# Kernel tuning notes

Measured on AMD Instinct MI355X. Metric: run time of the kernel, lower is better.

Reference implementation:

```python
import jax, jax.numpy as jnp
import numpy as np

B, N, QN, C, H = 4, 1024, 512, 1024, 16
D = C // H  # head_dim = 64


def setup_inputs() -> dict:
    key = jax.random.key(0)
    ks = jax.random.split(key, 8)
    w = lambda k, shape: jax.random.normal(k, shape, jnp.float32) * 0.02
    return dict(
        x=jax.random.normal(ks[0], (B, N, C), jnp.float32),
        query=jax.random.normal(ks[1], (B, QN, C), jnp.float32),
        w_qkv=w(ks[2], (3 * C, C)),        # self.qkv (no bias)
        w_kv=w(ks[3], (2 * C, C)),         # self.to_query_kv (no bias)
        w_qlin=w(ks[4], (3 * C, C)),       # self.query_linear (no bias)
        gate=jnp.zeros((1, H, 1, 1), jnp.float32),  # zero-initialized gate param
        w_proj=w(ks[5], (C, C)),
        b_proj=jnp.zeros((C,), jnp.float32),
        w_qproj=w(ks[6], (C, C)),
        b_qproj=jnp.zeros((C,), jnp.float32),
    )


def _sdpa(q, k, v, scale):
    # q,k,v: [B,H,S,D]; standard softmax attention (attn_mask=None, p=0)
    s = jnp.einsum('bhqd,bhkd->bhqk', q, k) * scale
    return jnp.einsum('bhqk,bhkd->bhqd', jax.nn.softmax(s, axis=-1), v)


def reference(x, query, w_qkv, w_kv, w_qlin, gate, w_proj, b_proj, w_qproj, b_qproj):
    scale = 1.0 / np.sqrt(D)
    # qkv on x -> [3,B,H,N,D]
    qkv = (x @ w_qkv.T).reshape(B, N, 3, H, D).transpose(2, 0, 3, 1, 4)
    q, k, v = qkv[0], qkv[1], qkv[2]
    # kv for cross path computed from ORIGINAL x (before self-attn), as in torch code
    kv = (x @ w_kv.T).reshape(B, N, 2, H, D).transpose(2, 0, 3, 1, 4)
    xk0, xv0 = kv[0], kv[1]
    # self-attention on x (x_mask=None)
    x_attn = _sdpa(q, k, v, scale)  # [B,H,N,D]
    # query qkv -> [3,B,H,QN,D]
    qq3 = (query @ w_qlin.T).reshape(B, QN, 3, H, D).transpose(2, 0, 3, 1, 4)
    qq, qk, qv = qq3[0], qq3[1], qq3[2]
    xk = jnp.concatenate([xk0, qk], axis=2)  # [B,H,N+QN,D]
    xv = jnp.concatenate([xv0, qv], axis=2)
    scores = jnp.einsum('bhqd,bhkd->bhqk', qq, xk) * scale  # [B,H,QN,N+QN]
    # split softmax with tanh-gated first segment (mask=None; dropout p=0)
    gated = jnp.concatenate(
        [jnp.tanh(gate) * jax.nn.softmax(scores[..., :N], axis=-1),
         jax.nn.softmax(scores[..., N:], axis=-1)], axis=-1)
    q_attn = jnp.einsum('bhqk,bhkd->bhqd', gated, xv)  # [B,H,QN,D]
    x_out = x_attn.transpose(0, 2, 1, 3).reshape(B, N, C) @ w_proj.T + b_proj
    q_out = q_attn.transpose(0, 2, 1, 3).reshape(B, QN, C) @ w_qproj.T + b_qproj
    return (x_out, q_out)
```

## Files before the change

### kernel.cpp

```cpp
#include <hip/hip_runtime.h>


using bf16 = __bf16;
typedef __bf16 bf16x4 __attribute__((ext_vector_type(4)));
typedef __bf16 bf16x8 __attribute__((ext_vector_type(8)));
typedef float  f32x4  __attribute__((ext_vector_type(4)));
typedef float  f32x16 __attribute__((ext_vector_type(16)));
typedef unsigned int u32x4 __attribute__((ext_vector_type(4)));

#define MFMA16(a, b, c) __builtin_amdgcn_mfma_f32_16x16x32_bf16((a), (b), (c), 0, 0, 0)
#define MFMA32(a, b, c) __builtin_amdgcn_mfma_f32_32x32x16_bf16((a), (b), (c), 0, 0, 0)

__device__ __forceinline__ int swz128(int row) { return ((row ^ (row >> 3)) & 7) << 4; }

__device__ __forceinline__ void gl_lds16(const void* g, void* l) {
  __builtin_amdgcn_global_load_lds(
      (const __attribute__((address_space(1))) unsigned int*)g,
      (__attribute__((address_space(3))) unsigned int*)l, 16, 0, 0);
}

__device__ __forceinline__ unsigned pack2(float a, float b) {
  unsigned short ua = __builtin_bit_cast(unsigned short, (bf16)a);
  unsigned short ub = __builtin_bit_cast(unsigned short, (bf16)b);
  return (unsigned)ua | ((unsigned)ub << 16);
}

__device__ __forceinline__ float exp2_fast(float x) {
  float r;
  asm("v_exp_f32 %0, %1" : "=v"(r) : "v"(x));
  return r;
}

#define WAITV(N) asm volatile("s_waitcnt vmcnt(" #N ")" ::: "memory")
#define RAW_BAR() do { __builtin_amdgcn_s_barrier(); asm volatile("" ::: "memory"); } while (0)

__global__ void k_cast_all(const float* __restrict__ s0, const float* __restrict__ s1,
                           const float* __restrict__ s2, const float* __restrict__ s3,
                           const float* __restrict__ s4, const float* __restrict__ s5,
                           const float* __restrict__ s6, bf16* __restrict__ dst) {
  constexpr size_t MM = 1u << 20;
  constexpr size_t o1 = 4 * MM, o2 = 6 * MM, o3 = 9 * MM, o4 = 11 * MM,
                   o5 = 14 * MM, o6 = 15 * MM, total = 16 * MM;
  size_t stride = (size_t)gridDim.x * blockDim.x * 8;
  for (size_t i = ((size_t)blockIdx.x * blockDim.x + threadIdx.x) * 8; i < total; i += stride) {
    const float* s; size_t loc;
    if (i < o1)      { s = s0; loc = i; }
    else if (i < o2) { s = s1; loc = i - o1; }
    else if (i < o3) { s = s2; loc = i - o2; }
    else if (i < o4) { s = s3; loc = i - o3; }
    else if (i < o5) { s = s4; loc = i - o4; }
    else if (i < o6) { s = s5; loc = i - o5; }
    else             { s = s6; loc = i - o6; }
    float4 a = *(const float4*)(s + loc);
    float4 b = *(const float4*)(s + loc + 4);
    bf16x8 o;
    o[0] = (bf16)a.x; o[1] = (bf16)a.y; o[2] = (bf16)a.z; o[3] = (bf16)a.w;
    o[4] = (bf16)b.x; o[5] = (bf16)b.y; o[6] = (bf16)b.z; o[7] = (bf16)b.w;
    *(bf16x8*)(dst + i) = o;
  }
}

__global__ __launch_bounds__(512, 2)
void k_gemm_big(const bf16* __restrict__ xb, const bf16* __restrict__ qb,
                const bf16* __restrict__ wqkvb, const bf16* __restrict__ wqlinb,
                bf16* __restrict__ XK, bf16* __restrict__ VTs, bf16* __restrict__ VT0,
                bf16* __restrict__ QQK, bf16* __restrict__ VTq) {
  constexpr int K = 1024, NK = 32;
  __shared__ bf16 As[3 * 256 * 32];
  __shared__ bf16 Bs[3 * 256 * 32];
  const int tid = threadIdx.x;
  const int lane = tid & 63, w = tid >> 6;
  const int wm = w >> 2, wn = w & 3;
  const int r0 = lane & 15, kg = lane >> 4;
  const int bid = ((int)blockIdx.x & 7) * 52 + ((int)blockIdx.x >> 3);
  int grp, tm, tn;
  const bf16 *Ap, *Bp;
  if (bid < 320) { grp = 0; tm = (bid / 20) * 256; tn = (bid % 20) * 256; Ap = xb; Bp = wqkvb; }
  else { grp = 1; int t = bid - 320; tm = (t / 12) * 256; tn = (t % 12) * 256; Ap = qb; Bp = wqlinb; }

  auto stage = [&](int step, int bi) {
    const int kk = step * 32;
#pragma unroll
    for (int j = 0; j < 2; j++) {
      int c = j * 512 + tid;
      int row = c >> 2, kb = c & 3;
      int sg = (kb ^ ((row >> 1) & 3)) * 8;
      gl_lds16(Ap + (size_t)(tm + row) * K + kk + sg, (char*)As + bi * 16384 + c * 16);
    }
#pragma unroll
    for (int j = 0; j < 2; j++) {
      int c = j * 512 + tid;
      int row = c >> 2, kb = c & 3;
      int sg = (kb ^ ((row >> 1) & 3)) * 8;
      gl_lds16(Bp + (size_t)(tn + row) * K + kk + sg, (char*)Bs + bi * 16384 + c * 16);
    }
  };

  f32x4 acc[8][4] = {};
  stage(0, 0);
  stage(1, 1);
  WAITV(4);
  RAW_BAR();

  for (int t = 0; t < NK; t++) {
    const int bi = t % 3;
    const bool more = (t + 2 < NK);
    if (more) stage(t + 2, (t + 2) % 3);
    const char* Ab = (const char*)As + bi * 16384;
    const char* Bb = (const char*)Bs + bi * 16384;
    bf16x8 af[8], bfv[4];
#pragma unroll
    for (int mf = 0; mf < 8; mf++) {
      int row = wm * 128 + mf * 16 + r0;
      af[mf] = *(const bf16x8*)(Ab + row * 64 + ((kg ^ ((row >> 1) & 3)) << 4));
    }
#pragma unroll
    for (int nf = 0; nf < 4; nf++) {
      int row = wn * 64 + nf * 16 + r0;
      bfv[nf] = *(const bf16x8*)(Bb + row * 64 + ((kg ^ ((row >> 1) & 3)) << 4));
    }
    __builtin_amdgcn_s_setprio(1);
#pragma unroll
    for (int mf = 0; mf < 8; mf++)
#pragma unroll
      for (int nf = 0; nf < 4; nf++)
        acc[mf][nf] = MFMA16(af[mf], bfv[nf], acc[mf][nf]);
    __builtin_amdgcn_s_setprio(0);
    if (more) { WAITV(4); } else { WAITV(0); }
    RAW_BAR();
  }

#pragma unroll
  for (int mf = 0; mf < 8; mf++) {
    const int rowb = tm + wm * 128 + mf * 16 + kg * 4;
#pragma unroll
    for (int nf = 0; nf < 4; nf++) {
      const int coln = tn + wn * 64 + nf * 16 + r0;
      bool rm; int rmcol = coln, vbase = 0, tokb = 10, rs_ = 3072;
      bf16* vt = VTs;
      bf16* rmp = XK;
      if (grp == 0) {
        if (tn < 2048)      { rm = true; }
        else if (tn < 3072) { rm = false; vbase = 2048; vt = VTs; }
        else if (tn < 4096) { rm = true; rmcol = coln - 1024; }
        else                { rm = false; vbase = 4096; vt = VT0; }
      } else {
        rs_ = 2048; tokb = 9; rmp = QQK;
        if (tn < 2048) { rm = true; }
        else           { rm = false; vbase = 2048; vt = VTq; }
      }
      if (rm) {
#pragma unroll
        for (int j = 0; j < 4; j++)
          rmp[(size_t)(rowb + j) * rs_ + rmcol] = (bf16)acc[mf][nf][j];
      } else {
        int dg = coln - vbase, h_ = dg >> 6, dd = dg & 63;
        int bq = rowb >> tokb, tok = rowb & ((1 << tokb) - 1);
        bf16x4 wv;
#pragma unroll
        for (int j = 0; j < 4; j++) wv[j] = (bf16)acc[mf][nf][j];
        *(bf16x4*)(vt + (((size_t)((bq * 16 + h_) * 64 + dd)) << tokb) + tok) = wv;
      }
    }
  }
}

__global__ __launch_bounds__(256)
void k_gemm_proj(const bf16* __restrict__ A, const bf16* __restrict__ B0,
                 const bf16* __restrict__ B1, const float* __restrict__ bias0,
                 const float* __restrict__ bias1, float* __restrict__ OUT) {
  constexpr int K = 1024, N = 1024;
  __shared__ bf16 As[128 * 64];
  __shared__ bf16 Bs[128 * 64];
  const int tid = threadIdx.x;
  const int lane = tid & 63, w = tid >> 6;
  const int wr = w >> 1, wc = w & 1;
  const int nbx = N / 128;
  const int bid = ((int)blockIdx.x & 7) * ((int)gridDim.x >> 3) + ((int)blockIdx.x >> 3);
  const int tm = (bid / nbx) * 128, tn = (bid % nbx) * 128;
  const int r0 = lane & 15, kg = lane >> 4;
  const bf16* Bp = (tm < 4096) ? B0 : B1;
  const float* bias = (tm < 4096) ? bias0 : bias1;
  f32x4 acc[4][4] = {};
  for (int kk = 0; kk < K; kk += 64) {
#pragma unroll
    for (int i = 0; i < 4; i++) {
      int c = i * 256 + tid;
      int row = c >> 3, kb = c & 7;
      int sb = (kb ^ ((row ^ (row >> 3)) & 7)) * 8;
      gl_lds16(A + (size_t)(tm + row) * K + kk + sb, (char*)As + c * 16);
      gl_lds16(Bp + (size_t)(tn + row) * K + kk + sb, (char*)Bs + c * 16);
    }
    __syncthreads();
#pragma unroll
    for (int ks = 0; ks < 2; ks++) {
      bf16x8 af[4], bfv[4];
#pragma unroll
      for (int f = 0; f < 4; f++) {
        int rowa = wr * 64 + f * 16 + r0;
        af[f] = *(const bf16x8*)((const char*)As +
                                 ((rowa * 128 + ks * 64 + kg * 16) ^ swz128(rowa)));
        int rowb = wc * 64 + f * 16 + r0;
        bfv[f] = *(const bf16x8*)((const char*)Bs +
                                  ((rowb * 128 + ks * 64 + kg * 16) ^ swz128(rowb)));
      }
#pragma unroll
      for (int mf = 0; mf < 4; mf++)
#pragma unroll
        for (int nf = 0; nf < 4; nf++)
          acc[mf][nf] = MFMA16(af[mf], bfv[nf], acc[mf][nf]);
    }
    __syncthreads();
  }
#pragma unroll
  for (int mf = 0; mf < 4; mf++)
#pragma unroll
    for (int j = 0; j < 4; j++) {
      int row = tm + wr * 64 + mf * 16 + kg * 4 + j;
#pragma unroll
      for (int nf = 0; nf < 4; nf++) {
        int col = tn + wc * 64 + nf * 16 + r0;
        OUT[(size_t)row * 1024 + col] = acc[mf][nf][j] + bias[col];
      }
    }
}

template<int NT>
__device__ __forceinline__ void attn_pass32(
    const bf16* __restrict__ Kg, int kRS,
    const bf16* __restrict__ VTg, int vRS,
    int ntiles, const bf16x8* qf, bf16* Ks, bf16* Vt,
    f32x16* o, float& m, float& rs) {
  const int tid = threadIdx.x;
  const int lane = tid & 63;
  const int lq = lane & 31, kg2 = lane >> 5;

  auto stage = [&](int t) {
    bf16* kd = Ks + (t % 3) * 4096;
    bf16* vd = Vt + (t % 3) * 4096;
    const bf16* kt = Kg + (size_t)t * 64 * kRS;
#pragma unroll
    for (int i = 0; i < 512 / NT; i++) {
      int c = i * NT + tid;
      int r = c >> 3, kb = c & 7;
      int sb = (kb ^ ((r ^ (r >> 3)) & 7)) * 8;
      gl_lds16(kt + (size_t)r * kRS + sb, (char*)kd + c * 16);
    }
#pragma unroll
    for (int i = 0; i < 512 / NT; i++) {
      int c = i * NT + tid;
      int r = c >> 3, kb = c & 7;
      int sb = (kb ^ ((r ^ (r >> 3)) & 7)) * 8;
      gl_lds16(VTg + (size_t)r * vRS + t * 64 + sb, (char*)vd + c * 16);
    }
  };

  stage(0);
  stage(1);
  WAITV(4);
  RAW_BAR();

  for (int t = 0; t < ntiles; t++) {
    const char* KsC = (const char*)(Ks + (t % 3) * 4096);
    const char* VtC = (const char*)(Vt + (t % 3) * 4096);
    const bool more = (t + 2 < ntiles);
    if (more) stage(t + 2);

    f32x16 s[2];
    s[0] = (f32x16)0.f; s[1] = (f32x16)0.f;
    __builtin_amdgcn_s_setprio(1);
#pragma unroll
    for (int kb = 0; kb < 2; kb++) {
      int row = kb * 32 + lq;
#pragma unroll
      for (int dw = 0; dw < 4; dw++) {
        bf16x8 kf = *(const bf16x8*)(KsC + ((row * 128 + dw * 32 + kg2 * 16) ^ swz128(row)));
        s[kb] = MFMA32(kf, qf[dw], s[kb]);
      }
    }
    __builtin_amdgcn_s_setprio(0);

    float vmax = s[0][0];
#pragma unroll
    for (int j = 1; j < 16; j++) vmax = fmaxf(vmax, s[0][j]);
#pragma unroll
    for (int j = 0; j < 16; j++) vmax = fmaxf(vmax, s[1][j]);
    vmax = fmaxf(vmax, __shfl_xor(vmax, 32, 64));
    if (__any(vmax > m + 11.5f)) {
      float mn = fmaxf(m, vmax);
      float fac = exp2_fast(m - mn);
      m = mn;
      rs *= fac;
#pragma unroll
      for (int j = 0; j < 16; j++) {
        int rowq = (j & 3) + 8 * (j >> 2) + 4 * kg2;
        float fj = __shfl(fac, rowq, 64);
        o[0][j] *= fj;
        o[1][j] *= fj;
      }
    }
    float tsum = 0.f;
    f32x16 p[2];
#pragma unroll
    for (int kb = 0; kb < 2; kb++)
#pragma unroll
      for (int j = 0; j < 16; j++) {
        float pv = exp2_fast(s[kb][j] - m);
        p[kb][j] = pv;
        tsum += pv;
      }
    tsum += __shfl_xor(tsum, 32, 64);
    rs += tsum;

    unsigned pk[2][4][2];
#pragma unroll
    for (int kb = 0; kb < 2; kb++)
#pragma unroll
      for (int n = 0; n < 4; n++) {
        pk[kb][n][0] = pack2(p[kb][4 * n + 0], p[kb][4 * n + 1]);
        pk[kb][n][1] = pack2(p[kb][4 * n + 2], p[kb][4 * n + 3]);
      }

#pragma unroll
    for (int w = 0; w < 4; w++) {
      const int kb = w >> 1, wb = w & 1;
      unsigned pushA = kg2 ? pk[kb][2 * wb][0] : pk[kb][2 * wb + 1][0];
      unsigned pushB = kg2 ? pk[kb][2 * wb][1] : pk[kb][2 * wb + 1][1];
      unsigned rcvA = __shfl_xor(pushA, 32, 64);
      unsigned rcvB = __shfl_xor(pushB, 32, 64);
      u32x4 fu;
      fu[0] = kg2 ? rcvA : pk[kb][2 * wb][0];
      fu[1] = kg2 ? rcvB : pk[kb][2 * wb][1];
      fu[2] = kg2 ? pk[kb][2 * wb + 1][0] : rcvA;
      fu[3] = kg2 ? pk[kb][2 * wb + 1][1] : rcvB;
      bf16x8 pfrag = __builtin_bit_cast(bf16x8, fu);
      __builtin_amdgcn_s_setprio(1);
#pragma unroll
      for (int db = 0; db < 2; db++) {
        int d = db * 32 + lq;
        bf16x8 vf = *(const bf16x8*)(VtC + ((d * 128 + w * 32 + kg2 * 16) ^ swz128(d)));
        o[db] = MFMA32(pfrag, vf, o[db]);
      }
      __builtin_amdgcn_s_setprio(0);
    }

    if (more) { WAITV(4); } else { WAITV(0); }
    RAW_BAR();
  }
}

__global__ __launch_bounds__(256)
void k_attn(const bf16* __restrict__ XK, const bf16* __restrict__ QQK,
            const bf16* __restrict__ VTs, const bf16* __restrict__ VT0,
            const bf16* __restrict__ VTq, const float* __restrict__ gate,
            bf16* __restrict__ xat, bf16* __restrict__ qat) {
  __shared__ bf16 Ks[3 * 4096], Vt[3 * 4096];
  const int pb = blockIdx.x;
  const int bid = (pb & 7) * 96 + (pb >> 3);
  const int bh = bid / 12, r = bid % 12;
  const int b = bh >> 4, h = bh & 15;
  const int tid = threadIdx.x, lane = tid & 63, wv = tid >> 6;
  const int lq = lane & 31, kg2 = lane >> 5;
  constexpr float QS = 0.125f * 1.44269504088896f;

  if (r < 8) {
    const int qtok = b * 1024 + r * 128 + wv * 32;
    bf16x8 qf[4];
#pragma unroll
    for (int dw = 0; dw < 4; dw++) {
      qf[dw] = *(const bf16x8*)(XK + (size_t)(qtok + lq) * 3072 + h * 64 + dw * 16 + kg2 * 8);
#pragma unroll
      for (int e = 0; e < 8; e++) qf[dw][e] = (bf16)((float)qf[dw][e] * QS);
    }
    f32x16 o[2];
    o[0] = (f32x16)0.f; o[1] = (f32x16)0.f;
    float m = -__builtin_inff(), rs = 0.f;
    attn_pass32<256>(XK + (size_t)(b * 1024) * 3072 + 1024 + h * 64, 3072,
                     VTs + (size_t)bh * 64 * 1024, 1024,
                     16, qf, Ks, Vt, o, m, rs);
#pragma unroll
    for (int j = 0; j < 16; j++) {
      int rowq = (j & 3) + 8 * (j >> 2) + 4 * kg2;
      float rsj = __shfl(rs, rowq, 64);
      size_t base = (size_t)(qtok + rowq) * 1024 + h * 64;
      xat[base + lq] = (bf16)(o[0][j] / rsj);
      xat[base + 32 + lq] = (bf16)(o[1][j] / rsj);
    }
  } else {
    const int qt = r - 8;
    const int qtok = b * 512 + qt * 128 + wv * 32;
    bf16x8 qf[4];
#pragma unroll
    for (int dw = 0; dw < 4; dw++) {
      qf[dw] = *(const bf16x8*)(QQK + (size_t)(qtok + lq) * 2048 + h * 64 + dw * 16 + kg2 * 8);
#pragma unroll
      for (int e = 0; e < 8; e++) qf[dw][e] = (bf16)((float)qf[dw][e] * QS);
    }
    const float g = tanhf(gate[h]);
    unsigned pka[2][8] = {};
    f32x16 o[2];
    o[0] = (f32x16)0.f; o[1] = (f32x16)0.f;
    float m, rs;
    if (g != 0.0f) {
      m = -__builtin_inff(); rs = 0.f;
      attn_pass32<256>(XK + (size_t)(b * 1024) * 3072 + 2048 + h * 64, 3072,
                       VT0 + (size_t)bh * 64 * 1024, 1024,
                       16, qf, Ks, Vt, o, m, rs);
#pragma unroll
      for (int j2 = 0; j2 < 8; j2++) {
        int j0 = 2 * j2;
        int rq0 = (j0 & 3) + 8 * (j0 >> 2) + 4 * kg2;
        float ra = __shfl(rs, rq0, 64);
        float rb = __shfl(rs, rq0 + 1, 64);
        pka[0][j2] = pack2(g * o[0][j0] / ra, g * o[0][j0 + 1] / rb);
        pka[1][j2] = pack2(g * o[1][j0] / ra, g * o[1][j0 + 1] / rb);
      }
      o[0] = (f32x16)0.f; o[1] = (f32x16)0.f;
    }
    m = -__builtin_inff(); rs = 0.f;
    attn_pass32<256>(QQK + (size_t)(b * 512) * 2048 + 1024 + h * 64, 2048,
                     VTq + (size_t)bh * 64 * 512, 512,
                     8, qf, Ks, Vt, o, m, rs);
#pragma unroll
    for (int j = 0; j < 16; j++) {
      int rowq = (j & 3) + 8 * (j >> 2) + 4 * kg2;
      float rsj = __shfl(rs, rowq, 64);
      size_t base = (size_t)(qtok + rowq) * 1024 + h * 64;
      unsigned wa = pka[0][j >> 1], wb = pka[1][j >> 1];
      unsigned short ua = (j & 1) ? (unsigned short)(wa >> 16) : (unsigned short)(wa & 0xffffu);
      unsigned short ub = (j & 1) ? (unsigned short)(wb >> 16) : (unsigned short)(wb & 0xffffu);
      float a0 = (float)__builtin_bit_cast(bf16, ua);
      float a1 = (float)__builtin_bit_cast(bf16, ub);
      qat[base + lq] = (bf16)(o[0][j] / rsj + a0);
      qat[base + 32 + lq] = (bf16)(o[1][j] / rsj + a1);
    }
  }
}

extern "C" void kernel_launch(void* const* d_in, const int* in_sizes, int n_in,
                              void* d_out, int out_size, void* d_ws, size_t ws_size,
                              hipStream_t stream) {
  (void)in_sizes; (void)n_in; (void)out_size; (void)ws_size;
  const float* x       = (const float*)d_in[0];
  const float* query   = (const float*)d_in[1];
  const float* w_qkv   = (const float*)d_in[2];
  const float* w_kv    = (const float*)d_in[3];
  const float* w_qlin  = (const float*)d_in[4];
  const float* gate    = (const float*)d_in[5];
  const float* w_proj  = (const float*)d_in[6];
  const float* b_proj  = (const float*)d_in[7];
  const float* w_qproj = (const float*)d_in[8];
  const float* b_qproj = (const float*)d_in[9];
  float* out = (float*)d_out;

  bf16* p = (bf16*)d_ws;
  bf16* xb = p;      p += (size_t)4096 * 1024;
  bf16* qb = p;      p += (size_t)2048 * 1024;
  bf16* wqkvb = p;   p += (size_t)3072 * 1024;
  bf16* wkvb = p;    p += (size_t)2048 * 1024;
  bf16* wqlinb = p;  p += (size_t)3072 * 1024;
  bf16* wprojb = p;  p += (size_t)1024 * 1024;
  bf16* wqprojb = p; p += (size_t)1024 * 1024;
  bf16* XK = p;      p += (size_t)4096 * 3072;
  bf16* VTs = p;     p += (size_t)64 * 64 * 1024;
  bf16* VT0 = p;     p += (size_t)64 * 64 * 1024;
  bf16* QQK = p;     p += (size_t)2048 * 2048;
  bf16* VTq = p;     p += (size_t)64 * 64 * 512;
  bf16* xat = p;     p += (size_t)4096 * 1024;
  bf16* qat = p;     p += (size_t)2048 * 1024;
  (void)wkvb;

  k_cast_all<<<2048, 256, 0, stream>>>(x, query, w_qkv, w_kv, w_qlin, w_proj, w_qproj,
                                       (bf16*)d_ws);

  k_gemm_big<<<dim3(416), 512, 0, stream>>>(xb, qb, wqkvb, wqlinb,
                                            XK, VTs, VT0, QQK, VTq);

  k_attn<<<dim3(768), 256, 0, stream>>>(XK, QQK, VTs, VT0, VTq, gate, xat, qat);

  k_gemm_proj<<<dim3(48 * 8), 256, 0, stream>>>(xat, wprojb, wqprojb, b_proj, b_qproj, out);
}
```

Baseline: 193.5 us.

## Restructure big GEMM mainloop into 4-phase half-tile pipeline with finer staging

Rewrites the QKV projection GEMM main loop to work on 64-wide K tiles, split into two 32-wide halves. Each iteration now runs four compute phases over half the M fragments. Each phase interleaves a quarter of the next stage's global-to-LDS loads with MFMA work, separated by barriers and lgkmcnt waits plus sched_barrier. The LDS buffering changes from triple-buffered 32-wide K slices to double-buffered 64-wide slices. The launch bound drops its min-blocks hint, which frees register allocation. The aim is to hide load latency and lower register pressure, at the cost of many more barriers per iteration and possibly reduced occupancy.

```diff
diff --git a/kernel.cpp b/kernel.cpp
--- a/kernel.cpp
+++ b/kernel.cpp
@@ -32,6 +32,8 @@
 }
 
 #define WAITV(N) asm volatile("s_waitcnt vmcnt(" #N ")" ::: "memory")
+#define LGKM0()  asm volatile("s_waitcnt lgkmcnt(0)" ::: "memory")
+#define SCHED0() __builtin_amdgcn_sched_barrier(0)
 #define RAW_BAR() do { __builtin_amdgcn_s_barrier(); asm volatile("" ::: "memory"); } while (0)
 
 __global__ void k_cast_all(const float* __restrict__ s0, const float* __restrict__ s1,
@@ -60,14 +62,14 @@
   }
 }
 
-__global__ __launch_bounds__(512, 2)
+__global__ __launch_bounds__(512)
 void k_gemm_big(const bf16* __restrict__ xb, const bf16* __restrict__ qb,
                 const bf16* __restrict__ wqkvb, const bf16* __restrict__ wqlinb,
                 bf16* __restrict__ XK, bf16* __restrict__ VTs, bf16* __restrict__ VT0,
                 bf16* __restrict__ QQK, bf16* __restrict__ VTq) {
-  constexpr int K = 1024, NK = 32;
-  __shared__ bf16 As[3 * 256 * 32];
-  __shared__ bf16 Bs[3 * 256 * 32];
+  constexpr int K = 1024, NT = 16;
+  __shared__ bf16 As[2 * 2 * 256 * 32];
+  __shared__ bf16 Bs[2 * 2 * 256 * 32];
   const int tid = threadIdx.x;
   const int lane = tid & 63, w = tid >> 6;
   const int wm = w >> 2, wn = w & 3;
@@ -78,55 +80,85 @@
   if (bid < 320) { grp = 0; tm = (bid / 20) * 256; tn = (bid % 20) * 256; Ap = xb; Bp = wqkvb; }
   else { grp = 1; int t = bid - 320; tm = (t / 12) * 256; tn = (t % 12) * 256; Ap = qb; Bp = wqlinb; }
 
-  auto stage = [&](int step, int bi) {
-    const int kk = step * 32;
-#pragma unroll
-    for (int j = 0; j < 2; j++) {
-      int c = j * 512 + tid;
-      int row = c >> 2, kb = c & 3;
-      int sg = (kb ^ ((row >> 1) & 3)) * 8;
-      gl_lds16(Ap + (size_t)(tm + row) * K + kk + sg, (char*)As + bi * 16384 + c * 16);
-    }
-#pragma unroll
-    for (int j = 0; j < 2; j++) {
-      int c = j * 512 + tid;
-      int row = c >> 2, kb = c & 3;
-      int sg = (kb ^ ((row >> 1) & 3)) * 8;
-      gl_lds16(Bp + (size_t)(tn + row) * K + kk + sg, (char*)Bs + bi * 16384 + c * 16);
+  auto stage = [&](int T, int mat, int kh) {
+    const bf16* src = mat ? Bp : Ap;
+    const int t0 = mat ? tn : tm;
+    char* base = (char*)(mat ? (void*)Bs : (void*)As) + (((T & 1) * 2 + kh) << 14);
+#pragma unroll
+    for (int i = 0; i < 2; i++) {
+      int c = i * 512 + tid;
+      int row = c >> 2, g = c & 3;
+      int sg = (g ^ ((row >> 1) & 3)) * 8;
+      gl_lds16(src + (size_t)(t0 + row) * K + T * 64 + kh * 32 + sg, base + c * 16);
     }
   };
+  auto ldA = [&](int bi, int kh, int row) -> bf16x8 {
+    return *(const bf16x8*)((const char*)As + ((bi * 2 + kh) << 14) + row * 64 +
+                            ((kg ^ ((row >> 1) & 3)) << 4));
+  };
+  auto ldB = [&](int bi, int kh, int row) -> bf16x8 {
+    return *(const bf16x8*)((const char*)Bs + ((bi * 2 + kh) << 14) + row * 64 +
+                            ((kg ^ ((row >> 1) & 3)) << 4));
+  };
 
   f32x4 acc[8][4] = {};
-  stage(0, 0);
-  stage(1, 1);
+
+  stage(0, 0, 0); stage(0, 1, 0); stage(0, 0, 1); stage(0, 1, 1);
+  stage(1, 0, 0); stage(1, 1, 0);
   WAITV(4);
   RAW_BAR();
 
-  for (int t = 0; t < NK; t++) {
-    const int bi = t % 3;
-    const bool more = (t + 2 < NK);
-    if (more) stage(t + 2, (t + 2) % 3);
-    const char* Ab = (const char*)As + bi * 16384;
-    const char* Bb = (const char*)Bs + bi * 16384;
-    bf16x8 af[8], bfv[4];
-#pragma unroll
-    for (int mf = 0; mf < 8; mf++) {
-      int row = wm * 128 + mf * 16 + r0;
-      af[mf] = *(const bf16x8*)(Ab + row * 64 + ((kg ^ ((row >> 1) & 3)) << 4));
-    }
-#pragma unroll
-    for (int nf = 0; nf < 4; nf++) {
-      int row = wn * 64 + nf * 16 + r0;
-      bfv[nf] = *(const bf16x8*)(Bb + row * 64 + ((kg ^ ((row >> 1) & 3)) << 4));
-    }
+  for (int j = 0; j < NT; ++j) {
+    const int bi = j & 1;
+    bf16x8 af[4], bfk[4];
+#pragma unroll
+    for (int i = 0; i < 4; i++) af[i] = ldA(bi, 0, wm * 128 + i * 16 + r0);
+#pragma unroll
+    for (int nf = 0; nf < 4; nf++) bfk[nf] = ldB(bi, 0, wn * 64 + nf * 16 + r0);
+    if (j + 1 < NT) stage(j + 1, 0, 1);
+    RAW_BAR(); LGKM0(); SCHED0();
     __builtin_amdgcn_s_setprio(1);
 #pragma unroll
-    for (int mf = 0; mf < 8; mf++)
-#pragma unroll
-      for (int nf = 0; nf < 4; nf++)
-        acc[mf][nf] = MFMA16(af[mf], bfv[nf], acc[mf][nf]);
+    for (int i = 0; i < 4; i++)
+#pragma unroll
+      for (int nf = 0; nf < 4; nf++) acc[i][nf] = MFMA16(af[i], bfk[nf], acc[i][nf]);
     __builtin_amdgcn_s_setprio(0);
-    if (more) { WAITV(4); } else { WAITV(0); }
+    RAW_BAR();
+#pragma unroll
+    for (int i = 0; i < 4; i++) af[i] = ldA(bi, 0, wm * 128 + 64 + i * 16 + r0);
+    if (j + 1 < NT) stage(j + 1, 1, 1);
+    RAW_BAR(); LGKM0(); SCHED0();
+    __builtin_amdgcn_s_setprio(1);
+#pragma unroll
+    for (int i = 0; i < 4; i++)
+#pragma unroll
+      for (int nf = 0; nf < 4; nf++) acc[4 + i][nf] = MFMA16(af[i], bfk[nf], acc[4 + i][nf]);
+    __builtin_amdgcn_s_setprio(0);
+    RAW_BAR();
+#pragma unroll
+    for (int i = 0; i < 4; i++) af[i] = ldA(bi, 1, wm * 128 + i * 16 + r0);
+#pragma unroll
+    for (int nf = 0; nf < 4; nf++) bfk[nf] = ldB(bi, 1, wn * 64 + nf * 16 + r0);
+    if (j + 2 < NT) stage(j + 2, 0, 0);
+    RAW_BAR(); LGKM0(); SCHED0();
+    __builtin_amdgcn_s_setprio(1);
+#pragma unroll
+    for (int i = 0; i < 4; i++)
+#pragma unroll
+      for (int nf = 0; nf < 4; nf++) acc[i][nf] = MFMA16(af[i], bfk[nf], acc[i][nf]);
+    __builtin_amdgcn_s_setprio(0);
+    RAW_BAR();
+#pragma unroll
+    for (int i = 0; i < 4; i++) af[i] = ldA(bi, 1, wm * 128 + 64 + i * 16 + r0);
+    if (j + 2 < NT) stage(j + 2, 1, 0);
+    RAW_BAR(); LGKM0(); SCHED0();
+    __builtin_amdgcn_s_setprio(1);
+#pragma unroll
+    for (int i = 0; i < 4; i++)
+#pragma unroll
+      for (int nf = 0; nf < 4; nf++) acc[4 + i][nf] = MFMA16(af[i], bfk[nf], acc[4 + i][nf]);
+    __builtin_amdgcn_s_setprio(0);
+    if (j < NT - 2) { WAITV(4); } else { WAITV(0); }
     RAW_BAR();
   }
 
```

Measured after the change: 179.6 us. 1.08x faster.
